# Performance work log

Measured on AMD Instinct MI355X. Metric: run time of the kernel, lower is better.

## Reference

```python
import jax, jax.numpy as jnp
import numpy as np

N_NODES = 10000
N_EDGES = 500000
IN_DIM = 512
HID = 256
VOCAB = 1000


def _gat(x, src, dst, W, a_src, a_dst, b, n):
    # PyG GATConv, heads=1: linear, per-edge attention logits,
    # segment softmax over target node, scatter-weighted-sum.
    h = x @ W                              # [N, C]
    e = jax.nn.leaky_relu(jnp.take(h @ a_src, src) + jnp.take(h @ a_dst, dst), 0.2)  # [E]
    m = jax.ops.segment_max(e, dst, num_segments=n)
    w = jnp.exp(e - m[dst])
    denom = jax.ops.segment_sum(w, dst, num_segments=n)
    alpha = w / denom[dst]                 # [E]
    out = jax.ops.segment_sum(alpha[:, None] * h[src], dst, num_segments=n)  # [N, C]
    return out + b


def _lstm(seq, W_ih, W_hh, b_ih, b_hh):
    # torch nn.LSTM single layer, gate order i,f,g,o; batch of 1 -> scan over nodes
    H = W_hh.shape[1]
    pre = seq @ W_ih.T + (b_ih + b_hh)     # [T, 4H] precomputed input projection

    def step(carry, xt):
        h, c = carry
        g = xt + h @ W_hh.T
        i, f, gg, o = jnp.split(g, 4)
        i = jax.nn.sigmoid(i); f = jax.nn.sigmoid(f)
        gg = jnp.tanh(gg); o = jax.nn.sigmoid(o)
        c = f * c + i * gg
        h = o * jnp.tanh(c)
        return (h, c), h

    init = (jnp.zeros((H,), seq.dtype), jnp.zeros((H,), seq.dtype))
    _, hs = jax.lax.scan(step, init, pre)
    return hs                               # [T, H]


def setup_inputs() -> dict:
    key = jax.random.key(0)
    ks = jax.random.split(key, 16)
    s = 0.05
    x = jax.random.normal(ks[0], (N_NODES, IN_DIM), jnp.float32)
    edge_index = jax.random.randint(ks[1], (2, N_EDGES), 0, N_NODES, jnp.int32)
    return {
        "x": x,
        "W1": jax.random.normal(ks[2], (IN_DIM, HID), jnp.float32) * s,
        "a_src1": jax.random.normal(ks[3], (HID,), jnp.float32) * s,
        "a_dst1": jax.random.normal(ks[4], (HID,), jnp.float32) * s,
        "b1": jnp.zeros((HID,), jnp.float32),
        "W2": jax.random.normal(ks[5], (HID, HID), jnp.float32) * s,
        "a_src2": jax.random.normal(ks[6], (HID,), jnp.float32) * s,
        "a_dst2": jax.random.normal(ks[7], (HID,), jnp.float32) * s,
        "b2": jnp.zeros((HID,), jnp.float32),
        "W_ih": jax.random.normal(ks[8], (4 * HID, HID), jnp.float32) * s,
        "W_hh": jax.random.normal(ks[9], (4 * HID, HID), jnp.float32) * s,
        "b_ih": jnp.zeros((4 * HID,), jnp.float32),
        "b_hh": jnp.zeros((4 * HID,), jnp.float32),
        "Wfc": jax.random.normal(ks[10], (VOCAB, HID), jnp.float32) * s,
        "bfc": jnp.zeros((VOCAB,), jnp.float32),
        "edge_index": edge_index,
    }


def reference(x, W1, a_src1, a_dst1, b1, W2, a_src2, a_dst2, b2,
              W_ih, W_hh, b_ih, b_hh, Wfc, bfc, edge_index):
    n = x.shape[0]
    loops = jnp.arange(n, dtype=edge_index.dtype)
    src = jnp.concatenate([edge_index[0], loops])  # PyG adds self-loops
    dst = jnp.concatenate([edge_index[1], loops])
    h = jax.nn.relu(_gat(x, src, dst, W1, a_src1, a_dst1, b1, n))
    h = _gat(h, src, dst, W2, a_src2, a_dst2, b2, n)
    hs = _lstm(h, W_ih, W_hh, b_ih, b_hh)          # [N, HID]
    logits = hs @ Wfc.T + bfc                      # [N, VOCAB]
    return logits
```

## Files before the change

### kernel.cpp

```cpp
#include <hip/hip_runtime.h>
#include <cstdint>

#define N_NODES 10000
#define N_EDGES 500000
#define E_TOT   510000
#define IN_DIM  512
#define HID     256
#define VOCAB   1000

typedef _Float16 h2v __attribute__((ext_vector_type(2)));

__device__ __forceinline__ float fdot2f(h2v a, h2v b, float c) {
#if __has_builtin(__builtin_amdgcn_fdot2)
    return __builtin_amdgcn_fdot2(a, b, c, false);
#else
    return c + (float)a[0] * (float)b[0] + (float)a[1] * (float)b[1];
#endif
}

__device__ __forceinline__ float sigmoidf_(float x) {
    return 1.f / (1.f + __expf(-x));
}
__device__ __forceinline__ float tanhf_(float x) {
    float ax = fabsf(x);
    float e  = __expf(-2.f * ax);
    float r  = (1.f - e) / (1.f + e);
    return x < 0.f ? -r : r;
}

template<bool TRANSB, int EPI>
__global__ __launch_bounds__(256) void gemm64(
    const float* __restrict__ A, const float* __restrict__ B,
    const float* __restrict__ bias, const float* __restrict__ bias2,
    float* __restrict__ C, int M, int N, int K, int ldc)
{
    __shared__ float As[16][68];
    __shared__ float Bs[16][68];
    const int tid = threadIdx.x;
    const int tx = tid & 15, ty = tid >> 4;
    const int m0 = blockIdx.x * 64, n0 = blockIdx.y * 64;
    float acc[4][4] = {};

    for (int k0 = 0; k0 < K; k0 += 16) {
        {
            int row = tid >> 2, col = (tid & 3) << 2;
            float4 v = make_float4(0.f, 0.f, 0.f, 0.f);
            if (m0 + row < M)
                v = *(const float4*)(A + (size_t)(m0 + row) * K + k0 + col);
            As[col + 0][row] = v.x; As[col + 1][row] = v.y;
            As[col + 2][row] = v.z; As[col + 3][row] = v.w;
        }
        if (!TRANSB) {
            int row = tid >> 4, col = (tid & 15) << 2;
            const float* bp = B + (size_t)(k0 + row) * N + n0 + col;
            float4 v = make_float4(0.f, 0.f, 0.f, 0.f);
            if (n0 + col + 3 < N) v = *(const float4*)bp;
            else {
                if (n0 + col + 0 < N) v.x = bp[0];
                if (n0 + col + 1 < N) v.y = bp[1];
                if (n0 + col + 2 < N) v.z = bp[2];
            }
            *(float4*)&Bs[row][col] = v;
        } else {
            int nr = tid >> 2, kc = (tid & 3) << 2;
            float4 v = make_float4(0.f, 0.f, 0.f, 0.f);
            if (n0 + nr < N)
                v = *(const float4*)(B + (size_t)(n0 + nr) * K + k0 + kc);
            Bs[kc + 0][nr] = v.x; Bs[kc + 1][nr] = v.y;
            Bs[kc + 2][nr] = v.z; Bs[kc + 3][nr] = v.w;
        }
        __syncthreads();
        #pragma unroll
        for (int kk = 0; kk < 16; ++kk) {
            float a[4], b[4];
            *(float4*)a = *(const float4*)&As[kk][ty << 2];
            *(float4*)b = *(const float4*)&Bs[kk][tx << 2];
            #pragma unroll
            for (int i = 0; i < 4; ++i)
                #pragma unroll
                for (int j = 0; j < 4; ++j)
                    acc[i][j] = fmaf(a[i], b[j], acc[i][j]);
        }
        __syncthreads();
    }
    #pragma unroll
    for (int i = 0; i < 4; ++i) {
        int m = m0 + (ty << 2) + i;
        if (m >= M) continue;
        #pragma unroll
        for (int j = 0; j < 4; ++j) {
            int n = n0 + (tx << 2) + j;
            if (n >= N) continue;
            float v = acc[i][j];
            if (bias)  v += bias[n];
            if (bias2) v += bias2[n];
            if (EPI == 1)
                C[(size_t)m * ldc + (((n & 255) << 2) + (n >> 8))] = v;
            else
                C[(size_t)m * ldc + n] = v;
        }
    }
}

__global__ __launch_bounds__(256) void scores_kernel(
    const float* __restrict__ H, const float* __restrict__ asrc,
    const float* __restrict__ adst, float* __restrict__ ssrc,
    float* __restrict__ sdst)
{
    int node = blockIdx.x * 4 + (threadIdx.x >> 6);
    int lane = threadIdx.x & 63;
    if (node >= N_NODES) return;
    float4 h = ((const float4*)H)[node * 64 + lane];
    float4 a = ((const float4*)asrc)[lane];
    float4 b = ((const float4*)adst)[lane];
    float ps = h.x * a.x + h.y * a.y + h.z * a.z + h.w * a.w;
    float pd = h.x * b.x + h.y * b.y + h.z * b.z + h.w * b.w;
    #pragma unroll
    for (int off = 32; off > 0; off >>= 1) {
        ps += __shfl_xor(ps, off);
        pd += __shfl_xor(pd, off);
    }
    if (lane == 0) { ssrc[node] = ps; sdst[node] = pd; }
}

__global__ __launch_bounds__(256) void edge_w_kernel(
    const int* __restrict__ ei, const float* __restrict__ ssrc,
    const float* __restrict__ sdst, float* __restrict__ wbuf,
    float* __restrict__ denom)
{
    int e = blockIdx.x * 256 + threadIdx.x;
    if (e >= E_TOT) return;
    int s, d;
    if (e < N_EDGES) { s = ei[e]; d = ei[N_EDGES + e]; }
    else             { s = d = e - N_EDGES; }
    float v = ssrc[s] + sdst[d];
    v = (v > 0.f) ? v : 0.2f * v;
    float w = __expf(v);
    wbuf[e] = w;
    unsafeAtomicAdd(&denom[d], w);
}

__global__ __launch_bounds__(256) void scatter_kernel(
    const int* __restrict__ ei, const float* __restrict__ H,
    const float* __restrict__ wbuf, float* __restrict__ S)
{
    int e = blockIdx.x * 4 + (threadIdx.x >> 6);
    int lane = threadIdx.x & 63;
    if (e >= E_TOT) return;
    int s, d;
    if (e < N_EDGES) { s = ei[e]; d = ei[N_EDGES + e]; }
    else             { s = d = e - N_EDGES; }
    float w = wbuf[e];
    float4 h = ((const float4*)H)[s * 64 + lane];
    float* outp = S + (size_t)d * HID + lane * 4;
    unsafeAtomicAdd(outp + 0, w * h.x);
    unsafeAtomicAdd(outp + 1, w * h.y);
    unsafeAtomicAdd(outp + 2, w * h.z);
    unsafeAtomicAdd(outp + 3, w * h.w);
}

__global__ __launch_bounds__(256) void finalize_kernel(
    const float* __restrict__ S, const float* __restrict__ denom,
    const float* __restrict__ bias, float* __restrict__ H, int relu)
{
    int idx = blockIdx.x * 256 + threadIdx.x;
    int n = idx >> 8, ci = idx & 255;
    float v = S[idx] / denom[n] + bias[ci];
    if (relu) v = fmaxf(v, 0.f);
    H[idx] = v;
}

__global__ __launch_bounds__(512, 2) void lstm_kernel(
    const float* __restrict__ Whh,
    const float* __restrict__ pre4,
    float* __restrict__ hs,
    int T)
{
    __shared__ uint4  oW4[512 * 16];
    __shared__ uint4  h4[32];
    __shared__ float4 pf4[512];

    const int t  = threadIdx.x;
    const int r0 = t & 255, s = t >> 8;
    const int sw = t & 7;

    h2v wi[64], wf[64], wg[64];
    {
        const float2* Wr = (const float2*)(Whh + (size_t)r0 * 256 + s * 128);
        #pragma unroll
        for (int j = 0; j < 64; ++j) {
            float2 v = Wr[j]; h2v w; w[0] = (_Float16)v.x; w[1] = (_Float16)v.y; wi[j] = w;
        }
        Wr = (const float2*)(Whh + (size_t)(r0 + 256) * 256 + s * 128);
        #pragma unroll
        for (int j = 0; j < 64; ++j) {
            float2 v = Wr[j]; h2v w; w[0] = (_Float16)v.x; w[1] = (_Float16)v.y; wf[j] = w;
        }
        Wr = (const float2*)(Whh + (size_t)(r0 + 512) * 256 + s * 128);
        #pragma unroll
        for (int j = 0; j < 64; ++j) {
            float2 v = Wr[j]; h2v w; w[0] = (_Float16)v.x; w[1] = (_Float16)v.y; wg[j] = w;
        }
        const float2* Wo = (const float2*)(Whh + (size_t)(r0 + 768) * 256 + s * 128);
        #pragma unroll
        for (int u = 0; u < 16; ++u) {
            unsigned int dd[4];
            #pragma unroll
            for (int q = 0; q < 4; ++q) {
                float2 v = Wo[u * 4 + q];
                h2v w; w[0] = (_Float16)v.x; w[1] = (_Float16)v.y;
                dd[q] = __builtin_bit_cast(unsigned int, w);
            }
            oW4[t * 16 + (u ^ sw)] = make_uint4(dd[0], dd[1], dd[2], dd[3]);
        }
    }
    if (t < 32) h4[t] = make_uint4(0, 0, 0, 0);
    float c = 0.f;
    float4 pren = make_float4(0.f, 0.f, 0.f, 0.f);
    if (t < 256) pren = ((const float4*)pre4)[t];
    __syncthreads();

    for (int step = 0; step < T; ++step) {
        float4 pnxt = pren;
        if (t < 256) {
            int ni = (step + 1 < T) ? (step + 1) : step;
            pnxt = ((const float4*)pre4)[(size_t)ni * 256 + t];
        }
        float ai = 0.f, af = 0.f, ag = 0.f, ao = 0.f;
        #pragma unroll
        for (int ch = 0; ch < 8; ++ch) {
            uint4 ha = h4[s * 16 + ch * 2 + 0];
            uint4 hb = h4[s * 16 + ch * 2 + 1];
            uint4 oa = oW4[t * 16 + ((ch * 2 + 0) ^ sw)];
            uint4 ob = oW4[t * 16 + ((ch * 2 + 1) ^ sw)];
            unsigned int hu[8] = {ha.x, ha.y, ha.z, ha.w, hb.x, hb.y, hb.z, hb.w};
            unsigned int ou[8] = {oa.x, oa.y, oa.z, oa.w, ob.x, ob.y, ob.z, ob.w};
            #pragma unroll
            for (int j = 0; j < 8; ++j) {
                h2v hh = __builtin_bit_cast(h2v, hu[j]);
                h2v oo = __builtin_bit_cast(h2v, ou[j]);
                ai = fdot2f(wi[ch * 8 + j], hh, ai);
                af = fdot2f(wf[ch * 8 + j], hh, af);
                ag = fdot2f(wg[ch * 8 + j], hh, ag);
                ao = fdot2f(oo,             hh, ao);
            }
        }
        pf4[t] = make_float4(ai, af, ag, ao);
        __syncthreads();
        if (t < 256) {
            float4 p0 = pf4[t], p1 = pf4[t + 256];
            float gi = p0.x + p1.x + pren.x;
            float gf = p0.y + p1.y + pren.y;
            float gg = p0.z + p1.z + pren.z;
            float go = p0.w + p1.w + pren.w;
            float i_ = sigmoidf_(gi);
            float f_ = sigmoidf_(gf);
            float g_ = tanhf_(gg);
            float o_ = sigmoidf_(go);
            c = fmaf(f_, c, i_ * g_);
            float hv = o_ * tanhf_(c);
            hs[(size_t)step * HID + t] = hv;
            ((_Float16*)h4)[t] = (_Float16)hv;
            pren = pnxt;
        }
        __syncthreads();
    }
}

extern "C" void kernel_launch(void* const* d_in, const int* in_sizes, int n_in,
                              void* d_out, int out_size, void* d_ws, size_t ws_size,
                              hipStream_t stream)
{
    const float* x   = (const float*)d_in[0];
    const float* W1  = (const float*)d_in[1];
    const float* as1 = (const float*)d_in[2];
    const float* ad1 = (const float*)d_in[3];
    const float* b1  = (const float*)d_in[4];
    const float* W2  = (const float*)d_in[5];
    const float* as2 = (const float*)d_in[6];
    const float* ad2 = (const float*)d_in[7];
    const float* b2  = (const float*)d_in[8];
    const float* Wih = (const float*)d_in[9];
    const float* Whh = (const float*)d_in[10];
    const float* bih = (const float*)d_in[11];
    const float* bhh = (const float*)d_in[12];
    const float* Wfc = (const float*)d_in[13];
    const float* bfc = (const float*)d_in[14];
    const int*   ei  = (const int*)d_in[15];
    float* out = (float*)d_out;

    float* ws    = (float*)d_ws;
    float* A     = ws;
    float* Bsc   = ws +  2560000;
    float* Cbuf  = ws +  5120000;
    float* pre   = ws +  7680000;
    float* wbuf  = ws + 17920000;
    float* denom = ws + 18430000;
    float* ssrc  = ws + 18440000;
    float* sdst  = ws + 18450000;

    dim3 blk(256);

    gemm64<false, 0><<<dim3(157, 4), blk, 0, stream>>>(
        x, W1, nullptr, nullptr, A, N_NODES, HID, IN_DIM, HID);
    scores_kernel<<<2500, blk, 0, stream>>>(A, as1, ad1, ssrc, sdst);
    hipMemsetAsync(Bsc, 0, (size_t)N_NODES * HID * 4, stream);
    hipMemsetAsync(denom, 0, (size_t)N_NODES * 4, stream);
    edge_w_kernel<<<(E_TOT + 255) / 256, blk, 0, stream>>>(ei, ssrc, sdst, wbuf, denom);
    scatter_kernel<<<E_TOT / 4, blk, 0, stream>>>(ei, A, wbuf, Bsc);
    finalize_kernel<<<N_NODES, blk, 0, stream>>>(Bsc, denom, b1, Cbuf, 1);

    gemm64<false, 0><<<dim3(157, 4), blk, 0, stream>>>(
        Cbuf, W2, nullptr, nullptr, A, N_NODES, HID, HID, HID);
    scores_kernel<<<2500, blk, 0, stream>>>(A, as2, ad2, ssrc, sdst);
    hipMemsetAsync(Bsc, 0, (size_t)N_NODES * HID * 4, stream);
    hipMemsetAsync(denom, 0, (size_t)N_NODES * 4, stream);
    edge_w_kernel<<<(E_TOT + 255) / 256, blk, 0, stream>>>(ei, ssrc, sdst, wbuf, denom);
    scatter_kernel<<<E_TOT / 4, blk, 0, stream>>>(ei, A, wbuf, Bsc);
    finalize_kernel<<<N_NODES, blk, 0, stream>>>(Bsc, denom, b2, Cbuf, 0);

    gemm64<true, 1><<<dim3(157, 16), blk, 0, stream>>>(
        Cbuf, Wih, bih, bhh, pre, N_NODES, 4 * HID, HID, 4 * HID);
    lstm_kernel<<<1, 512, 0, stream>>>(Whh, pre, A, N_NODES);

    gemm64<true, 0><<<dim3(157, 16), blk, 0, stream>>>(
        A, Wfc, bfc, nullptr, out, N_NODES, VOCAB, HID, VOCAB);
}
```

Baseline: 18.61 ms.

## Compute LSTM recurrent matvec with MFMA and split weights across registers, LDS, global

After: 26.61 ms. 42.9% more time.

```diff
diff --git a/kernel.cpp b/kernel.cpp
--- a/kernel.cpp
+++ b/kernel.cpp
@@ -8,15 +8,9 @@
 #define HID     256
 #define VOCAB   1000
 
-typedef _Float16 h2v __attribute__((ext_vector_type(2)));
-
-__device__ __forceinline__ float fdot2f(h2v a, h2v b, float c) {
-#if __has_builtin(__builtin_amdgcn_fdot2)
-    return __builtin_amdgcn_fdot2(a, b, c, false);
-#else
-    return c + (float)a[0] * (float)b[0] + (float)a[1] * (float)b[1];
-#endif
-}
+typedef _Float16 h2v   __attribute__((ext_vector_type(2)));
+typedef _Float16 half8v __attribute__((ext_vector_type(8)));
+typedef float    f32x4v __attribute__((ext_vector_type(4)));
 
 __device__ __forceinline__ float sigmoidf_(float x) {
     return 1.f / (1.f + __expf(-x));
@@ -26,6 +20,10 @@
     float e  = __expf(-2.f * ax);
     float r  = (1.f - e) / (1.f + e);
     return x < 0.f ? -r : r;
+}
+
+__device__ __forceinline__ f32x4v mfma16(half8v a, half8v b, f32x4v c) {
+    return __builtin_amdgcn_mfma_f32_16x16x32_f16(a, b, c, 0, 0, 0);
 }
 
 template<bool TRANSB, int EPI>
@@ -174,85 +172,89 @@
     const float* __restrict__ Whh,
     const float* __restrict__ pre4,
     float* __restrict__ hs,
+    uint4* __restrict__ gp,
     int T)
 {
-    __shared__ uint4  oW4[512 * 16];
-    __shared__ uint4  h4[32];
-    __shared__ float4 pf4[512];
-
-    const int t  = threadIdx.x;
-    const int r0 = t & 255, s = t >> 8;
-    const int sw = t & 7;
-
-    h2v wi[64], wf[64], wg[64];
-    {
-        const float2* Wr = (const float2*)(Whh + (size_t)r0 * 256 + s * 128);
+    __shared__ uint4 sfrag[14 * 512];
+    __shared__ float ybuf[1024];
+    __shared__ __align__(16) _Float16 hbuf[256];
+
+    const int t     = threadIdx.x;
+    const int l     = t & 63;
+    const int w     = t >> 6;
+    const int row16 = l & 15;
+    const int kq    = l >> 4;
+    const int R0    = w * 128;
+
+    half8v Ar[40];
+    #pragma unroll
+    for (int kt = 0; kt < 8; ++kt) {
         #pragma unroll
-        for (int j = 0; j < 64; ++j) {
-            float2 v = Wr[j]; h2v w; w[0] = (_Float16)v.x; w[1] = (_Float16)v.y; wi[j] = w;
-        }
-        Wr = (const float2*)(Whh + (size_t)(r0 + 256) * 256 + s * 128);
-        #pragma unroll
-        for (int j = 0; j < 64; ++j) {
-            float2 v = Wr[j]; h2v w; w[0] = (_Float16)v.x; w[1] = (_Float16)v.y; wf[j] = w;
-        }
-        Wr = (const float2*)(Whh + (size_t)(r0 + 512) * 256 + s * 128);
-        #pragma unroll
-        for (int j = 0; j < 64; ++j) {
-            float2 v = Wr[j]; h2v w; w[0] = (_Float16)v.x; w[1] = (_Float16)v.y; wg[j] = w;
-        }
-        const float2* Wo = (const float2*)(Whh + (size_t)(r0 + 768) * 256 + s * 128);
-        #pragma unroll
-        for (int u = 0; u < 16; ++u) {
-            unsigned int dd[4];
+        for (int rt = 0; rt < 8; ++rt) {
+            const float* src = Whh + (size_t)(R0 + rt * 16 + row16) * 256
+                                   + kt * 32 + kq * 8;
+            half8v v;
             #pragma unroll
-            for (int q = 0; q < 4; ++q) {
-                float2 v = Wo[u * 4 + q];
-                h2v w; w[0] = (_Float16)v.x; w[1] = (_Float16)v.y;
-                dd[q] = __builtin_bit_cast(unsigned int, w);
-            }
-            oW4[t * 16 + (u ^ sw)] = make_uint4(dd[0], dd[1], dd[2], dd[3]);
-        }
-    }
-    if (t < 32) h4[t] = make_uint4(0, 0, 0, 0);
+            for (int e = 0; e < 8; ++e) v[e] = (_Float16)src[e];
+            if (kt < 5)                 Ar[kt * 8 + rt] = v;
+            else if (kt == 5)           sfrag[rt * 512 + t]       = __builtin_bit_cast(uint4, v);
+            else if (kt == 6 && rt < 6) sfrag[(8 + rt) * 512 + t] = __builtin_bit_cast(uint4, v);
+            else if (kt == 6)           gp[(rt - 6) * 512 + t]    = __builtin_bit_cast(uint4, v);
+            else                        gp[(2 + rt) * 512 + t]    = __builtin_bit_cast(uint4, v);
+        }
+    }
+    if (t < 256) hbuf[t] = (_Float16)0.f;
     float c = 0.f;
-    float4 pren = make_float4(0.f, 0.f, 0.f, 0.f);
-    if (t < 256) pren = ((const float4*)pre4)[t];
     __syncthreads();
 
+#define SF(fi) __builtin_bit_cast(half8v, sfrag[(fi) * 512 + t])
+#define GV(n)  __builtin_bit_cast(half8v, g##n)
+#define KT_BLOCK(kt, A0, A1, A2, A3, A4, A5, A6, A7)                         \
+    { half8v Bf = __builtin_bit_cast(half8v,                                 \
+          *(const uint4*)(hbuf + (kt) * 32 + kq * 8));                       \
+      C[0] = mfma16(A0, Bf, C[0]); C[1] = mfma16(A1, Bf, C[1]);              \
+      C[2] = mfma16(A2, Bf, C[2]); C[3] = mfma16(A3, Bf, C[3]);              \
+      C[4] = mfma16(A4, Bf, C[4]); C[5] = mfma16(A5, Bf, C[5]);              \
+      C[6] = mfma16(A6, Bf, C[6]); C[7] = mfma16(A7, Bf, C[7]); }
+
     for (int step = 0; step < T; ++step) {
-        float4 pnxt = pren;
+        float4 pre = make_float4(0.f, 0.f, 0.f, 0.f);
+        if (t < 256) pre = ((const float4*)pre4)[(size_t)step * 256 + t];
+
+        uint4 g0 = gp[0 * 512 + t], g1 = gp[1 * 512 + t];
+        uint4 g2 = gp[2 * 512 + t], g3 = gp[3 * 512 + t];
+        uint4 g4 = gp[4 * 512 + t], g5 = gp[5 * 512 + t];
+        uint4 g6 = gp[6 * 512 + t], g7 = gp[7 * 512 + t];
+        uint4 g8 = gp[8 * 512 + t], g9 = gp[9 * 512 + t];
+
+        f32x4v C[8];
+        {
+            f32x4v z = {0.f, 0.f, 0.f, 0.f};
+            #pragma unroll
+            for (int rt = 0; rt < 8; ++rt) C[rt] = z;
+        }
+
+        KT_BLOCK(0, Ar[0],  Ar[1],  Ar[2],  Ar[3],  Ar[4],  Ar[5],  Ar[6],  Ar[7])
+        KT_BLOCK(1, Ar[8],  Ar[9],  Ar[10], Ar[11], Ar[12], Ar[13], Ar[14], Ar[15])
+        KT_BLOCK(2, Ar[16], Ar[17], Ar[18], Ar[19], Ar[20], Ar[21], Ar[22], Ar[23])
+        KT_BLOCK(3, Ar[24], Ar[25], Ar[26], Ar[27], Ar[28], Ar[29], Ar[30], Ar[31])
+        KT_BLOCK(4, Ar[32], Ar[33], Ar[34], Ar[35], Ar[36], Ar[37], Ar[38], Ar[39])
+        KT_BLOCK(5, SF(0),  SF(1),  SF(2),  SF(3),  SF(4),  SF(5),  SF(6),  SF(7))
+        KT_BLOCK(6, SF(8),  SF(9),  SF(10), SF(11), SF(12), SF(13), GV(0),  GV(1))
+        KT_BLOCK(7, GV(2),  GV(3),  GV(4),  GV(5),  GV(6),  GV(7),  GV(8),  GV(9))
+
+        if (row16 == 0) {
+            #pragma unroll
+            for (int rt = 0; rt < 8; ++rt)
+                *(float4*)&ybuf[R0 + rt * 16 + kq * 4] = *(float4*)&C[rt];
+        }
+        __syncthreads();
+
         if (t < 256) {
-            int ni = (step + 1 < T) ? (step + 1) : step;
-            pnxt = ((const float4*)pre4)[(size_t)ni * 256 + t];
-        }
-        float ai = 0.f, af = 0.f, ag = 0.f, ao = 0.f;
-        #pragma unroll
-        for (int ch = 0; ch < 8; ++ch) {
-            uint4 ha = h4[s * 16 + ch * 2 + 0];
-            uint4 hb = h4[s * 16 + ch * 2 + 1];
-            uint4 oa = oW4[t * 16 + ((ch * 2 + 0) ^ sw)];
-            uint4 ob = oW4[t * 16 + ((ch * 2 + 1) ^ sw)];
-            unsigned int hu[8] = {ha.x, ha.y, ha.z, ha.w, hb.x, hb.y, hb.z, hb.w};
-            unsigned int ou[8] = {oa.x, oa.y, oa.z, oa.w, ob.x, ob.y, ob.z, ob.w};
-            #pragma unroll
-            for (int j = 0; j < 8; ++j) {
-                h2v hh = __builtin_bit_cast(h2v, hu[j]);
-                h2v oo = __builtin_bit_cast(h2v, ou[j]);
-                ai = fdot2f(wi[ch * 8 + j], hh, ai);
-                af = fdot2f(wf[ch * 8 + j], hh, af);
-                ag = fdot2f(wg[ch * 8 + j], hh, ag);
-                ao = fdot2f(oo,             hh, ao);
-            }
-        }
-        pf4[t] = make_float4(ai, af, ag, ao);
-        __syncthreads();
-        if (t < 256) {
-            float4 p0 = pf4[t], p1 = pf4[t + 256];
-            float gi = p0.x + p1.x + pren.x;
-            float gf = p0.y + p1.y + pren.y;
-            float gg = p0.z + p1.z + pren.z;
-            float go = p0.w + p1.w + pren.w;
+            float gi = ybuf[t]       + pre.x;
+            float gf = ybuf[256 + t] + pre.y;
+            float gg = ybuf[512 + t] + pre.z;
+            float go = ybuf[768 + t] + pre.w;
             float i_ = sigmoidf_(gi);
             float f_ = sigmoidf_(gf);
             float g_ = tanhf_(gg);
@@ -260,11 +262,13 @@
             c = fmaf(f_, c, i_ * g_);
             float hv = o_ * tanhf_(c);
             hs[(size_t)step * HID + t] = hv;
-            ((_Float16*)h4)[t] = (_Float16)hv;
-            pren = pnxt;
+            hbuf[t] = (_Float16)hv;
         }
         __syncthreads();
     }
+#undef SF
+#undef GV
+#undef KT_BLOCK
 }
 
 extern "C" void kernel_launch(void* const* d_in, const int* in_sizes, int n_in,
@@ -321,7 +325,7 @@
 
     gemm64<true, 1><<<dim3(157, 16), blk, 0, stream>>>(
         Cbuf, Wih, bih, bhh, pre, N_NODES, 4 * HID, HID, 4 * HID);
-    lstm_kernel<<<1, 512, 0, stream>>>(Whh, pre, A, N_NODES);
+    lstm_kernel<<<1, 512, 0, stream>>>(Whh, pre, A, (uint4*)Bsc, N_NODES);
 
     gemm64<true, 0><<<dim3(157, 16), blk, 0, stream>>>(
         A, Wfc, bfc, nullptr, out, N_NODES, VOCAB, HID, VOCAB);
```
